# Performance work log

Measured on AMD Instinct MI355X. Metric: run time of the kernel, lower is better.

## Reference

```python
import jax, jax.numpy as jnp
import numpy as np
import math

B, S, HID, NH = 2, 2048, 1024, 16
HD = HID // NH  # head_dim = 64
TEMPERATURE = 1.0


def setup_inputs() -> dict:
    key = jax.random.key(0)
    ks = jax.random.split(key, 6)
    w = lambda k: (jax.random.normal(k, (HID, HID), dtype=jnp.float32) * 0.02)
    return {
        "hidden_states": jax.random.normal(ks[0], (B, S, HID), dtype=jnp.float32),
        "attention_mask": jnp.ones((B, S), dtype=jnp.float32),
        "Wq": w(ks[1]), "bq": jnp.zeros((HID,), jnp.float32),
        "Wk": w(ks[2]), "bk": jnp.zeros((HID,), jnp.float32),
        "Wv": w(ks[3]), "bv": jnp.zeros((HID,), jnp.float32),
        "Wo": w(ks[4]), "bo": jnp.zeros((HID,), jnp.float32),
    }


def reference(hidden_states, attention_mask, Wq, bq, Wk, bk, Wv, bv, Wo, bo):
    b, s, hid = hidden_states.shape
    heads = lambda x: x.reshape(b, s, NH, HD).transpose(0, 2, 1, 3)  # [b,h,s,d]

    q = heads(hidden_states @ Wq.T + bq)
    k = heads(hidden_states @ Wk.T + bk)
    v = heads(hidden_states @ Wv.T + bv)

    # padding mask applied multiplicatively to k and v
    m = attention_mask[:, None, :, None]  # [b,1,s,1]
    k = k * m
    v = v * m

    # auxiliary Hopfield state: k^T @ v per head -> [b,h,d,d]
    state = jnp.einsum("bhsd,bhse->bhde", k, v)

    # energy / scores
    energy = jnp.einsum("bhqd,bhkd->bhqk", q, k) / (TEMPERATURE * math.sqrt(HD))
    causal = jnp.triu(jnp.ones((s, s), dtype=bool), k=1)  # True above diagonal
    energy = jnp.where(causal[None, None], -jnp.inf, energy)
    energy = jnp.where(attention_mask[:, None, None, :] == 0, -jnp.inf, energy)

    attn = jax.nn.softmax(energy, axis=-1)
    out = jnp.einsum("bhqk,bhkd->bhqd", attn, v)
    out = out.transpose(0, 2, 1, 3).reshape(b, s, hid)
    out = out @ Wo.T + bo
    return out, state
```

## Files before the change

kernel.cpp:

```cpp
#include <hip/hip_runtime.h>
#include <hip/hip_bf16.h>

#define B_ 2
#define S_ 2048
#define HID_ 1024
#define NH_ 16
#define HD_ 64
#define MTOK (B_*S_)
#define LDQKV 3072
#define SCALE_LOG2E 0.18033688011112043f

typedef __attribute__((ext_vector_type(8))) __bf16 bf16x8;
typedef __attribute__((ext_vector_type(4))) __bf16 bf16x4;
typedef __attribute__((ext_vector_type(4))) float f32x4;

__device__ __forceinline__ void gl16(__bf16* lds, const __bf16* g) {
  __builtin_amdgcn_global_load_lds(
      (const __attribute__((address_space(1))) void*)g,
      (__attribute__((address_space(3))) void*)lds, 16, 0, 0);
}

__device__ __forceinline__ int gswz(int row) { return ((row ^ (row >> 2)) & 3) << 4; }

__global__ __launch_bounds__(256) void cast_all(
    const float* __restrict__ X,
    const float* __restrict__ Wq, const float* __restrict__ Wk,
    const float* __restrict__ Wv, const float* __restrict__ Wo,
    __bf16* __restrict__ Xb, __bf16* __restrict__ Wqkvb, __bf16* __restrict__ Wob)
{
  const int base = blockIdx.x * 256 + threadIdx.x;
  #pragma unroll
  for (int k = 0; k < 4; k++) {
    int i = base + k * 524288;
    const float* src; __bf16* dst; int j;
    if (i < (1 << 20))              { src = X;  dst = Xb;                 j = i; }
    else if (i < (1<<20)+(1<<18))   { src = Wq; dst = Wqkvb;              j = i - (1<<20); }
    else if (i < (1<<20)+(2<<18))   { src = Wk; dst = Wqkvb + (1<<20);    j = i - (1<<20) - (1<<18); }
    else if (i < (1<<20)+(3<<18))   { src = Wv; dst = Wqkvb + (2<<20);    j = i - (1<<20) - (2<<18); }
    else                            { src = Wo; dst = Wob;                j = i - (1<<20) - (3<<18); }
    float4 v = reinterpret_cast<const float4*>(src)[j];
    bf16x4 o;
    o[0] = (__bf16)v.x; o[1] = (__bf16)v.y; o[2] = (__bf16)v.z; o[3] = (__bf16)v.w;
    reinterpret_cast<bf16x4*>(dst)[j] = o;
  }
}

__global__ __launch_bounds__(256) void gemm_qkv(
    const __bf16* __restrict__ A, const __bf16* __restrict__ W,
    const float* __restrict__ bq, const float* __restrict__ bk,
    const float* __restrict__ bv, const float* __restrict__ mask,
    __bf16* __restrict__ C)
{
  __shared__ __bf16 SM[24576];
  const int t = threadIdx.x;
  const int m0 = blockIdx.y * 128;
  const int n0 = blockIdx.x * 128;
  const int lane = t & 63;
  const int w = t >> 6;
  const int wr = (w >> 1) * 64;
  const int wc = (w & 1) * 64;
  const int fr = lane & 15;
  const int kg = lane >> 4;

  f32x4 acc[4][4];
  #pragma unroll
  for (int i = 0; i < 4; i++)
    #pragma unroll
    for (int j = 0; j < 4; j++) acc[i][j] = (f32x4)0.f;

  const int srow = w * 16 + (lane >> 2);
  const int scolb = ((lane & 3) * 16) ^ gswz(srow);
  const __bf16* ap0 = A + (size_t)(m0 + srow) * HID_ + (scolb >> 1);
  const __bf16* ap1 = A + (size_t)(m0 + 64 + srow) * HID_ + (scolb >> 1);
  const __bf16* wp0 = W + (size_t)(n0 + srow) * HID_ + (scolb >> 1);
  const __bf16* wp1 = W + (size_t)(n0 + 64 + srow) * HID_ + (scolb >> 1);

  #define STAGE3(buf, koff) { \
    __bf16* ab = SM + (buf) * 4096; \
    __bf16* bb = SM + 12288 + (buf) * 4096; \
    gl16(ab + w * 512, ap0 + (koff)); \
    gl16(ab + 2048 + w * 512, ap1 + (koff)); \
    gl16(bb + w * 512, wp0 + (koff)); \
    gl16(bb + 2048 + w * 512, wp1 + (koff)); }

  STAGE3(0, 0);
  STAGE3(1, 32);
  int bc = 0, bp2 = 2;
  for (int step = 0; step < 32; ++step) {
    if (step + 1 < 32) { asm volatile("s_waitcnt vmcnt(4)" ::: "memory"); }
    else               { asm volatile("s_waitcnt vmcnt(0)" ::: "memory"); }
    __builtin_amdgcn_sched_barrier(0);
    __builtin_amdgcn_s_barrier();
    if (step + 2 < 32) STAGE3(bp2, (step + 2) * 32);

    const __bf16* ab = SM + bc * 4096;
    const __bf16* bb = SM + 12288 + bc * 4096;
    bf16x8 af[4], bf[4];
    #pragma unroll
    for (int m = 0; m < 4; m++) {
      int row = wr + m*16 + fr;
      af[m] = *(const bf16x8*)((const char*)ab + row * 64 + ((kg * 16) ^ gswz(row)));
    }
    #pragma unroll
    for (int n = 0; n < 4; n++) {
      int row = wc + n*16 + fr;
      bf[n] = *(const bf16x8*)((const char*)bb + row * 64 + ((kg * 16) ^ gswz(row)));
    }
    #pragma unroll
    for (int m = 0; m < 4; m++)
      #pragma unroll
      for (int n = 0; n < 4; n++)
        acc[m][n] = __builtin_amdgcn_mfma_f32_16x16x32_bf16(af[m], bf[n], acc[m][n], 0, 0, 0);

    bc = (bc == 2) ? 0 : bc + 1;
    bp2 = (bp2 == 2) ? 0 : bp2 + 1;
  }

  const int region = n0 >> 10;
  const float* bias = region == 0 ? bq : (region == 1 ? bk : bv);
  const int nloc = n0 & 1023;

  #pragma unroll
  for (int m = 0; m < 4; m++) {
    #pragma unroll
    for (int r = 0; r < 4; r++) {
      int row = m0 + wr + m*16 + kg*4 + r;
      float rs = region ? mask[row] : SCALE_LOG2E;
      #pragma unroll
      for (int n = 0; n < 4; n++) {
        int c = wc + n*16 + fr;
        C[(size_t)row * LDQKV + n0 + c] = (__bf16)((acc[m][n][r] + bias[nloc + c]) * rs);
      }
    }
  }
}

__global__ __launch_bounds__(256) void transpose_kv(
    const __bf16* __restrict__ Kin, const __bf16* __restrict__ Vin,
    __bf16* __restrict__ Kt, __bf16* __restrict__ Vt)
{
  __shared__ __bf16 tile[64][68];
  const int tok0 = blockIdx.x * 64;
  const int f0 = blockIdx.y * 64;
  const __bf16* in = blockIdx.z ? Vin : Kin;
  __bf16* out = blockIdx.z ? Vt : Kt;
  const int t = threadIdx.x;
  const int r = t >> 2;
  const int c0 = (t & 3) * 16;
  const __bf16* src = in + (size_t)(tok0 + r) * LDQKV + f0 + c0;
  *(bf16x8*)&tile[r][c0]     = *(const bf16x8*)src;
  *(bf16x8*)&tile[r][c0 + 8] = *(const bf16x8*)(src + 8);
  __syncthreads();
  bf16x8 o0, o1;
  #pragma unroll
  for (int j = 0; j < 8; j++) { o0[j] = tile[c0 + j][r]; o1[j] = tile[c0 + 8 + j][r]; }
  __bf16* dst = out + (size_t)(f0 + r) * MTOK + tok0 + c0;
  *(bf16x8*)dst = o0;
  *(bf16x8*)(dst + 8) = o1;
}

__global__ __launch_bounds__(256) void gemm_o(
    const __bf16* __restrict__ A, const __bf16* __restrict__ W,
    const float* __restrict__ bias, const float* __restrict__ part,
    float* __restrict__ C)
{
  if (blockIdx.y >= 32) {
    const int bl = blockIdx.x + (blockIdx.y - 32) * 8;
    const int tid = bl * 256 + threadIdx.x;
    float* outState = C + (size_t)MTOK * HID_;
    #pragma unroll 4
    for (int e = 0; e < 32; e++) {
      int i = e * 4096 + tid;
      int bh = i >> 12, de = i & 4095;
      float s = 0.f;
      #pragma unroll
      for (int sc = 0; sc < 8; sc++) s += part[(size_t)((bh << 3) + sc) * 4096 + de];
      outState[i] = s;
    }
    return;
  }

  __shared__ __bf16 SM[24576];
  const int t = threadIdx.x;
  const int m0 = blockIdx.y * 128;
  const int n0 = blockIdx.x * 128;
  const int lane = t & 63;
  const int w = t >> 6;
  const int wr = (w >> 1) * 64;
  const int wc = (w & 1) * 64;
  const int fr = lane & 15;
  const int kg = lane >> 4;

  f32x4 acc[4][4];
  #pragma unroll
  for (int i = 0; i < 4; i++)
    #pragma unroll
    for (int j = 0; j < 4; j++) acc[i][j] = (f32x4)0.f;

  const int srow = w * 16 + (lane >> 2);
  const int scolb = ((lane & 3) * 16) ^ gswz(srow);
  const __bf16* ap0 = A + (size_t)(m0 + srow) * HID_ + (scolb >> 1);
  const __bf16* ap1 = A + (size_t)(m0 + 64 + srow) * HID_ + (scolb >> 1);
  const __bf16* wp0 = W + (size_t)(n0 + srow) * HID_ + (scolb >> 1);
  const __bf16* wp1 = W + (size_t)(n0 + 64 + srow) * HID_ + (scolb >> 1);

  STAGE3(0, 0);
  STAGE3(1, 32);
  int bc = 0, bp2 = 2;
  for (int step = 0; step < 32; ++step) {
    if (step + 1 < 32) { asm volatile("s_waitcnt vmcnt(4)" ::: "memory"); }
    else               { asm volatile("s_waitcnt vmcnt(0)" ::: "memory"); }
    __builtin_amdgcn_sched_barrier(0);
    __builtin_amdgcn_s_barrier();
    if (step + 2 < 32) STAGE3(bp2, (step + 2) * 32);

    const __bf16* ab = SM + bc * 4096;
    const __bf16* bb = SM + 12288 + bc * 4096;
    bf16x8 af[4], bf[4];
    #pragma unroll
    for (int m = 0; m < 4; m++) {
      int row = wr + m*16 + fr;
      af[m] = *(const bf16x8*)((const char*)ab + row * 64 + ((kg * 16) ^ gswz(row)));
    }
    #pragma unroll
    for (int n = 0; n < 4; n++) {
      int row = wc + n*16 + fr;
      bf[n] = *(const bf16x8*)((const char*)bb + row * 64 + ((kg * 16) ^ gswz(row)));
    }
    #pragma unroll
    for (int m = 0; m < 4; m++)
      #pragma unroll
      for (int n = 0; n < 4; n++)
        acc[m][n] = __builtin_amdgcn_mfma_f32_16x16x32_bf16(af[m], bf[n], acc[m][n], 0, 0, 0);

    bc = (bc == 2) ? 0 : bc + 1;
    bp2 = (bp2 == 2) ? 0 : bp2 + 1;
  }

  #pragma unroll
  for (int m = 0; m < 4; m++) {
    #pragma unroll
    for (int r = 0; r < 4; r++) {
      int row = m0 + wr + m*16 + kg*4 + r;
      #pragma unroll
      for (int n = 0; n < 4; n++) {
        int col = n0 + wc + n*16 + fr;
        C[(size_t)row * HID_ + col] = acc[m][n][r] + bias[col];
      }
    }
  }
}

__device__ __forceinline__ bf16x8 ld_swz(const __bf16* base, int row, int xb) {
  return *(const bf16x8*)((const char*)base + row * 128 + (xb ^ ((row & 7) << 4)));
}
__device__ __forceinline__ void st_swz16(__bf16* base, int row, int colbyte, __bf16 v) {
  *(__bf16*)((char*)base + row * 128 + (colbyte ^ ((row & 7) << 4))) = v;
}
__device__ __forceinline__ bf16x8 ld_swz256(const __bf16* base, int row, int xb) {
  return *(const bf16x8*)((const char*)base + row * 256 + (xb ^ ((row & 7) << 4)));
}

__device__ __forceinline__ void attn_tile(
    const __bf16* __restrict__ ks, const __bf16* __restrict__ vs,
    const bool (&okm)[4], __bf16* __restrict__ pw,
    const bf16x8 (&qa)[2], f32x4 (&acc)[4], f32x4& accl,
    const bf16x8 ones, int q0w, int kt, int fc, int kg)
{
  f32x4 s[4];
  #pragma unroll
  for (int n = 0; n < 4; n++) s[n] = (f32x4)0.f;
  __builtin_amdgcn_s_setprio(1);
  #pragma unroll
  for (int kd = 0; kd < 2; kd++)
    #pragma unroll
    for (int n = 0; n < 4; n++) {
      bf16x8 kf = ld_swz(ks, n * 16 + fc, kd * 64 + kg * 16);
      s[n] = __builtin_amdgcn_mfma_f32_16x16x32_bf16(qa[kd], kf, s[n], 0, 0, 0);
    }
  __builtin_amdgcn_s_setprio(0);

  const int g4 = kg * 4;
  const bool fullt = (kt * 64 + 63 <= q0w);
  if (fullt) {
    #pragma unroll
    for (int r = 0; r < 4; r++)
      #pragma unroll
      for (int n = 0; n < 4; n++) {
        float p = okm[n] ? __builtin_amdgcn_exp2f(s[n][r]) : 0.f;
        st_swz16(pw, g4 + r, (n * 16 + fc) * 2, (__bf16)p);
      }
  } else {
    #pragma unroll
    for (int r = 0; r < 4; r++) {
      const int qg = q0w + g4 + r;
      #pragma unroll
      for (int n = 0; n < 4; n++) {
        bool ok = okm[n] && (kt * 64 + n * 16 + fc <= qg);
        float p = ok ? __builtin_amdgcn_exp2f(s[n][r]) : 0.f;
        st_swz16(pw, g4 + r, (n * 16 + fc) * 2, (__bf16)p);
      }
    }
  }

  __builtin_amdgcn_s_setprio(1);
  #pragma unroll
  for (int kc = 0; kc < 2; kc++) {
    bf16x8 pf = ld_swz(pw, fc, kc * 64 + kg * 16);
    accl = __builtin_amdgcn_mfma_f32_16x16x32_bf16(pf, ones, accl, 0, 0, 0);
    #pragma unroll
    for (int n = 0; n < 4; n++) {
      bf16x8 vf = ld_swz(vs, n * 16 + fc, kc * 64 + kg * 16);
      acc[n] = __builtin_amdgcn_mfma_f32_16x16x32_bf16(pf, vf, acc[n], 0, 0, 0);
    }
  }
  __builtin_amdgcn_s_setprio(0);
}

__global__ __launch_bounds__(256) void flash_state(
    const __bf16* __restrict__ Q, const __bf16* __restrict__ K,
    const __bf16* __restrict__ Vt, const float* __restrict__ mask,
    __bf16* __restrict__ O, const __bf16* __restrict__ Kt,
    float* __restrict__ part)
{
  __shared__ __bf16 SMEM[16384];

  const int t = threadIdx.x;
  const int w = t >> 6;
  const int lane = t & 63;
  const int fc = lane & 15;
  const int kg = lane >> 4;

  if (blockIdx.y >= 32) {
    const int bh = blockIdx.x, sc = blockIdx.y - 32;
    const int b = bh >> 4, h = bh & 15;
    __bf16* Kl = &SMEM[0];
    __bf16* Vl = &SMEM[8192];
    const int rloc = lane >> 4;
    const int cb = (lane & 15) * 16;

    f32x4 acc[4];
    #pragma unroll
    for (int n = 0; n < 4; n++) acc[n] = (f32x4)0.f;

    for (int ch = 0; ch < 2; ch++) {
      const size_t colbase = (size_t)b * S_ + sc * 256 + ch * 128;
      __syncthreads();
      #pragma unroll
      for (int c = 0; c < 4; c++) {
        int row = w * 16 + c * 4 + rloc;
        int scol = (cb ^ ((row & 7) << 4)) >> 1;
        gl16(&Kl[(w * 16 + c * 4) * 128], Kt + (size_t)(h * HD_ + row) * MTOK + colbase + scol);
        gl16(&Vl[(w * 16 + c * 4) * 128], Vt + (size_t)(h * HD_ + row) * MTOK + colbase + scol);
      }
      __syncthreads();

      #pragma unroll
      for (int ks = 0; ks < 4; ks++) {
        bf16x8 af = ld_swz256(Kl, w * 16 + fc, ks * 64 + kg * 16);
        #pragma unroll
        for (int n = 0; n < 4; n++) {
          bf16x8 bfr = ld_swz256(Vl, n * 16 + fc, ks * 64 + kg * 16);
          acc[n] = __builtin_amdgcn_mfma_f32_16x16x32_bf16(af, bfr, acc[n], 0, 0, 0);
        }
      }
    }

    float* dst = part + ((size_t)((bh << 3) + sc) << 12);
    #pragma unroll
    for (int n = 0; n < 4; n++)
      #pragma unroll
      for (int r = 0; r < 4; r++)
        dst[(w * 16 + kg * 4 + r) * 64 + n * 16 + fc] = acc[n][r];
    return;
  }

  const int bh = blockIdx.x;
  const int ya = (int)blockIdx.y & 7;
  const int yg = (int)blockIdx.y >> 3;
  const int qt = (yg == 0) ? 31 - ya : (yg == 1) ? 16 + ya
               : (yg == 2) ? 15 - ya : ya;
  const int b = bh >> 4, h = bh & 15;
  const int g4 = kg * 4;

  const int q0w = qt * 64 + w * 16;
  const size_t tokbase = (size_t)b * S_;

  const int rr = lane >> 3;
  const int cswz = ((lane & 7) ^ rr) * 8;
  const int ktmax = qt;

  __bf16* Vsb = &SMEM[8192];
  __bf16* pw = &SMEM[12288 + w * 1024];

  bf16x8 qa[2];
  {
    const __bf16* qp = Q + (tokbase + q0w + fc) * LDQKV + h * HD_;
    qa[0] = *(const bf16x8*)(qp + kg * 8);
    qa[1] = *(const bf16x8*)(qp + 32 + kg * 8);
  }

  const __bf16* kp0 = K + (tokbase + (size_t)(w * 16 + rr)) * LDQKV + h * HD_ + cswz;
  const __bf16* kp1 = kp0 + (size_t)8 * LDQKV;
  const __bf16* vp0 = Vt + (size_t)(h * HD_ + w * 16 + rr) * MTOK + tokbase + cswz;
  const __bf16* vp1 = vp0 + (size_t)8 * MTOK;

  gl16(&SMEM[(w * 16) * 64],     kp0);
  gl16(&SMEM[(w * 16 + 8) * 64], kp1);
  kp0 += (size_t)64 * LDQKV; kp1 += (size_t)64 * LDQKV;
  gl16(&Vsb[(w * 16) * 64],     vp0);
  gl16(&Vsb[(w * 16 + 8) * 64], vp1);
  vp0 += 64; vp1 += 64;

  const float* mp = mask + tokbase + fc;
  float mnxt[4];
  #pragma unroll
  for (int n = 0; n < 4; n++) mnxt[n] = mp[n * 16];

  bf16x8 ones;
  #pragma unroll
  for (int j = 0; j < 8; j++) ones[j] = (__bf16)1.f;

  f32x4 acc[4], accl;
  #pragma unroll
  for (int n = 0; n < 4; n++) acc[n] = (f32x4)0.f;
  accl = (f32x4)0.f;

  for (int kt = 0; kt <= ktmax; ++kt) {
    float mcur[4];
    #pragma unroll
    for (int n = 0; n < 4; n++) mcur[n] = mnxt[n];

    if (kt < ktmax) {
      #pragma unroll
      for (int n = 0; n < 4; n++) mnxt[n] = mp[(kt + 1) * 64 + n * 16];
      __bf16* kb = &SMEM[((kt + 1) & 1) * 4096];
      gl16(&kb[(w * 16) * 64],     kp0);
      gl16(&kb[(w * 16 + 8) * 64], kp1);
      kp0 += (size_t)64 * LDQKV; kp1 += (size_t)64 * LDQKV;
      asm volatile("s_waitcnt vmcnt(6)" ::: "memory");
    } else {
      asm volatile("s_waitcnt vmcnt(0)" ::: "memory");
    }
    __builtin_amdgcn_sched_barrier(0);
    __builtin_amdgcn_s_barrier();

    bool okm[4];
    #pragma unroll
    for (int n = 0; n < 4; n++) okm[n] = (mcur[n] != 0.f);

    attn_tile(&SMEM[(kt & 1) * 4096], Vsb, okm, pw, qa, acc, accl, ones, q0w, kt, fc, kg);

    __builtin_amdgcn_s_barrier();

    if (kt < ktmax) {
      gl16(&Vsb[(w * 16) * 64],     vp0);
      gl16(&Vsb[(w * 16 + 8) * 64], vp1);
      vp0 += 64; vp1 += 64;
    }
  }

  #pragma unroll
  for (int r = 0; r < 4; r++) {
    float inv = accl[r] > 0.f ? 1.f / accl[r] : 0.f;
    __bf16* op = O + (tokbase + q0w + g4 + r) * HID_ + h * HD_;
    #pragma unroll
    for (int n = 0; n < 4; n++)
      op[n * 16 + fc] = (__bf16)(acc[n][r] * inv);
  }
}

extern "C" void kernel_launch(void* const* d_in, const int* in_sizes, int n_in,
                              void* d_out, int out_size, void* d_ws, size_t ws_size,
                              hipStream_t stream)
{
  const float* hs   = (const float*)d_in[0];
  const float* mask = (const float*)d_in[1];
  const float* Wq   = (const float*)d_in[2];
  const float* bq   = (const float*)d_in[3];
  const float* Wk   = (const float*)d_in[4];
  const float* bk   = (const float*)d_in[5];
  const float* Wv   = (const float*)d_in[6];
  const float* bv   = (const float*)d_in[7];
  const float* Wo   = (const float*)d_in[8];
  const float* bo   = (const float*)d_in[9];
  float* out = (float*)d_out;

  char* ws = (char*)d_ws;
  __bf16* Wqkvb = (__bf16*)(ws);
  __bf16* Wob   = (__bf16*)(ws + (6u  << 20));
  __bf16* Xb    = (__bf16*)(ws + (8u  << 20));
  __bf16* QKV   = (__bf16*)(ws + (16u << 20));
  __bf16* Ob    = (__bf16*)(ws + (40u << 20));
  __bf16* Ktg   = (__bf16*)(ws + (48u << 20));

  cast_all<<<2048, 256, 0, stream>>>(hs, Wq, Wk, Wv, Wo, Xb, Wqkvb, Wob);

  gemm_qkv<<<dim3(LDQKV / 128, MTOK / 128), 256, 0, stream>>>(
      Xb, Wqkvb, bq, bk, bv, mask, QKV);

  __bf16* Vtg = Xb;
  transpose_kv<<<dim3(MTOK / 64, HID_ / 64, 2), 256, 0, stream>>>(
      QKV + 1024, QKV + 2048, Ktg, Vtg);

  float* part = (float*)Wqkvb;

  flash_state<<<dim3(B_ * NH_, 40), 256, 0, stream>>>(
      QKV, QKV + 1024, Vtg, mask, Ob, Ktg, part);

  gemm_o<<<dim3(HID_ / 128, 34), 256, 0, stream>>>(Ob, Wob, bo, part, out);
}
```

Baseline: 119.4 us.

## Fuse K/V transpose into QKV GEMM epilogue and drop transpose kernel

```diff
diff --git a/kernel.cpp b/kernel.cpp
--- a/kernel.cpp
+++ b/kernel.cpp
@@ -7,7 +7,7 @@
 #define NH_ 16
 #define HD_ 64
 #define MTOK (B_*S_)
-#define LDQKV 3072
+#define LDQK 2048
 #define SCALE_LOG2E 0.18033688011112043f
 
 typedef __attribute__((ext_vector_type(8))) __bf16 bf16x8;
@@ -49,7 +49,7 @@
     const __bf16* __restrict__ A, const __bf16* __restrict__ W,
     const float* __restrict__ bq, const float* __restrict__ bk,
     const float* __restrict__ bv, const float* __restrict__ mask,
-    __bf16* __restrict__ C)
+    __bf16* __restrict__ C, __bf16* __restrict__ Kt, __bf16* __restrict__ Vt)
 {
   __shared__ __bf16 SM[24576];
   const int t = threadIdx.x;
@@ -117,9 +117,29 @@
   }
 
   const int region = n0 >> 10;
-  const float* bias = region == 0 ? bq : (region == 1 ? bk : bv);
   const int nloc = n0 & 1023;
 
+  if (region == 2) {
+    #pragma unroll
+    for (int m = 0; m < 4; m++) {
+      const int tok0 = m0 + wr + m*16 + kg*4;
+      float rs0 = mask[tok0], rs1 = mask[tok0+1], rs2 = mask[tok0+2], rs3 = mask[tok0+3];
+      #pragma unroll
+      for (int n = 0; n < 4; n++) {
+        int c = nloc + wc + n*16 + fr;
+        float bb_ = bv[c];
+        bf16x4 o;
+        o[0] = (__bf16)((acc[m][n][0] + bb_) * rs0);
+        o[1] = (__bf16)((acc[m][n][1] + bb_) * rs1);
+        o[2] = (__bf16)((acc[m][n][2] + bb_) * rs2);
+        o[3] = (__bf16)((acc[m][n][3] + bb_) * rs3);
+        *(bf16x4*)(Vt + (size_t)c * MTOK + tok0) = o;
+      }
+    }
+    return;
+  }
+
+  const float* bias = region == 0 ? bq : bk;
   #pragma unroll
   for (int m = 0; m < 4; m++) {
     #pragma unroll
@@ -129,34 +149,29 @@
       #pragma unroll
       for (int n = 0; n < 4; n++) {
         int c = wc + n*16 + fr;
-        C[(size_t)row * LDQKV + n0 + c] = (__bf16)((acc[m][n][r] + bias[nloc + c]) * rs);
-      }
-    }
-  }
-}
-
-__global__ __launch_bounds__(256) void transpose_kv(
-    const __bf16* __restrict__ Kin, const __bf16* __restrict__ Vin,
-    __bf16* __restrict__ Kt, __bf16* __restrict__ Vt)
-{
-  __shared__ __bf16 tile[64][68];
-  const int tok0 = blockIdx.x * 64;
-  const int f0 = blockIdx.y * 64;
-  const __bf16* in = blockIdx.z ? Vin : Kin;
-  __bf16* out = blockIdx.z ? Vt : Kt;
-  const int t = threadIdx.x;
-  const int r = t >> 2;
-  const int c0 = (t & 3) * 16;
-  const __bf16* src = in + (size_t)(tok0 + r) * LDQKV + f0 + c0;
-  *(bf16x8*)&tile[r][c0]     = *(const bf16x8*)src;
-  *(bf16x8*)&tile[r][c0 + 8] = *(const bf16x8*)(src + 8);
-  __syncthreads();
-  bf16x8 o0, o1;
-  #pragma unroll
-  for (int j = 0; j < 8; j++) { o0[j] = tile[c0 + j][r]; o1[j] = tile[c0 + 8 + j][r]; }
-  __bf16* dst = out + (size_t)(f0 + r) * MTOK + tok0 + c0;
-  *(bf16x8*)dst = o0;
-  *(bf16x8*)(dst + 8) = o1;
+        C[(size_t)row * LDQK + n0 + c] = (__bf16)((acc[m][n][r] + bias[nloc + c]) * rs);
+      }
+    }
+  }
+
+  if (region == 1) {
+    #pragma unroll
+    for (int m = 0; m < 4; m++) {
+      const int tok0 = m0 + wr + m*16 + kg*4;
+      float rs0 = mask[tok0], rs1 = mask[tok0+1], rs2 = mask[tok0+2], rs3 = mask[tok0+3];
+      #pragma unroll
+      for (int n = 0; n < 4; n++) {
+        int c = nloc + wc + n*16 + fr;
+        float bb_ = bk[c];
+        bf16x4 o;
+        o[0] = (__bf16)((acc[m][n][0] + bb_) * rs0);
+        o[1] = (__bf16)((acc[m][n][1] + bb_) * rs1);
+        o[2] = (__bf16)((acc[m][n][2] + bb_) * rs2);
+        o[3] = (__bf16)((acc[m][n][3] + bb_) * rs3);
+        *(bf16x4*)(Kt + (size_t)c * MTOK + tok0) = o;
+      }
+    }
+  }
 }
 
 __global__ __launch_bounds__(256) void gemm_o(
@@ -395,19 +410,19 @@
 
   bf16x8 qa[2];
   {
-    const __bf16* qp = Q + (tokbase + q0w + fc) * LDQKV + h * HD_;
+    const __bf16* qp = Q + (tokbase + q0w + fc) * LDQK + h * HD_;
     qa[0] = *(const bf16x8*)(qp + kg * 8);
     qa[1] = *(const bf16x8*)(qp + 32 + kg * 8);
   }
 
-  const __bf16* kp0 = K + (tokbase + (size_t)(w * 16 + rr)) * LDQKV + h * HD_ + cswz;
-  const __bf16* kp1 = kp0 + (size_t)8 * LDQKV;
+  const __bf16* kp0 = K + (tokbase + (size_t)(w * 16 + rr)) * LDQK + h * HD_ + cswz;
+  const __bf16* kp1 = kp0 + (size_t)8 * LDQK;
   const __bf16* vp0 = Vt + (size_t)(h * HD_ + w * 16 + rr) * MTOK + tokbase + cswz;
   const __bf16* vp1 = vp0 + (size_t)8 * MTOK;
 
   gl16(&SMEM[(w * 16) * 64],     kp0);
   gl16(&SMEM[(w * 16 + 8) * 64], kp1);
-  kp0 += (size_t)64 * LDQKV; kp1 += (size_t)64 * LDQKV;
+  kp0 += (size_t)64 * LDQK; kp1 += (size_t)64 * LDQK;
   gl16(&Vsb[(w * 16) * 64],     vp0);
   gl16(&Vsb[(w * 16 + 8) * 64], vp1);
   vp0 += 64; vp1 += 64;
@@ -437,7 +452,7 @@
       __bf16* kb = &SMEM[((kt + 1) & 1) * 4096];
       gl16(&kb[(w * 16) * 64],     kp0);
       gl16(&kb[(w * 16 + 8) * 64], kp1);
-      kp0 += (size_t)64 * LDQKV; kp1 += (size_t)64 * LDQKV;
+      kp0 += (size_t)64 * LDQK; kp1 += (size_t)64 * LDQK;
       asm volatile("s_waitcnt vmcnt(6)" ::: "memory");
     } else {
       asm volatile("s_waitcnt vmcnt(0)" ::: "memory");
@@ -490,23 +505,20 @@
   __bf16* Wqkvb = (__bf16*)(ws);
   __bf16* Wob   = (__bf16*)(ws + (6u  << 20));
   __bf16* Xb    = (__bf16*)(ws + (8u  << 20));
-  __bf16* QKV   = (__bf16*)(ws + (16u << 20));
+  __bf16* QK    = (__bf16*)(ws + (16u << 20));
+  __bf16* Vtg   = (__bf16*)(ws + (32u << 20));
   __bf16* Ob    = (__bf16*)(ws + (40u << 20));
   __bf16* Ktg   = (__bf16*)(ws + (48u << 20));
 
   cast_all<<<2048, 256, 0, stream>>>(hs, Wq, Wk, Wv, Wo, Xb, Wqkvb, Wob);
 
-  gemm_qkv<<<dim3(LDQKV / 128, MTOK / 128), 256, 0, stream>>>(
-      Xb, Wqkvb, bq, bk, bv, mask, QKV);
-
-  __bf16* Vtg = Xb;
-  transpose_kv<<<dim3(MTOK / 64, HID_ / 64, 2), 256, 0, stream>>>(
-      QKV + 1024, QKV + 2048, Ktg, Vtg);
+  gemm_qkv<<<dim3(3072 / 128, MTOK / 128), 256, 0, stream>>>(
+      Xb, Wqkvb, bq, bk, bv, mask, QK, Ktg, Vtg);
 
   float* part = (float*)Wqkvb;
 
   flash_state<<<dim3(B_ * NH_, 40), 256, 0, stream>>>(
-      QKV, QKV + 1024, Vtg, mask, Ob, Ktg, part);
+      QK, QK + 1024, Vtg, mask, Ob, Ktg, part);
 
   gemm_o<<<dim3(HID_ / 128, 34), 256, 0, stream>>>(Ob, Wob, bo, part, out);
 }
```

Result: no change. 119.1 us (-0.3%).
